# Kernel tuning notes

Hardware: AMD Instinct MI355X
Metric: run time of the kernel (lower is better)

## Reference

```python
import jax, jax.numpy as jnp
import numpy as np

B, H, S, F_RANK, D_HEAD = 1, 8, 4096, 64, 64
NEG = -1e9


def setup_inputs() -> dict:
    key = jax.random.key(0)
    k1, k2, k3, k4 = jax.random.split(key, 4)
    v = jax.random.normal(k1, (B, H, S, D_HEAD), dtype=jnp.float32)
    A1 = jax.random.normal(k2, (B, H, S, F_RANK), dtype=jnp.float32)
    A2 = jax.random.normal(k3, (B, H, F_RANK, S), dtype=jnp.float32)
    mask = jax.random.randint(k4, (B, 1, S, S), 0, 2, dtype=jnp.int32)
    return {"v": v, "A1": A1, "A2": A2, "mask": mask, "len_q": S}


def reference(v, A1, A2, mask, len_q):
    # Rank-f factorized scores: [B,H,len_q,len_q]
    scores = jnp.einsum('bhsf,bhft->bhst', A1[:, :, :len_q, :], A2[:, :, :, :len_q])
    scores = scores[:mask.shape[0]]
    # masked_fill(mask != 0, -1e9)
    scores = jnp.where(mask[:, :, :len_q, :len_q] != 0, jnp.float32(NEG), scores)
    attn = jax.nn.softmax(scores, axis=-1)  # dropout is identity in eval mode
    output = jnp.einsum('bhst,bhtd->bhsd', attn, v[:, :, :len_q, :])
    return (output, attn)
```

## Files before the change

### kernel.cpp

```cpp
#include <hip/hip_runtime.h>
#include <hip/hip_bf16.h>
#include <stdint.h>

#define S_LEN 4096
#define NHEAD 8
#define L2E   1.44269504088896340736f

typedef __attribute__((ext_vector_type(8))) short bf16x8;
typedef __attribute__((ext_vector_type(4))) float f32x4;
typedef unsigned short u16;
typedef unsigned int   u32;

#define MFMA16(a,b,c) __builtin_amdgcn_mfma_f32_16x16x32_bf16((a),(b),(c),0,0,0)
#define EXP2F(x) __builtin_amdgcn_exp2f((x))

__device__ __forceinline__ void gl_lds16(const void* g, void* l) {
  __builtin_amdgcn_global_load_lds((const __attribute__((address_space(1))) void*)g,
                                   (__attribute__((address_space(3))) void*)l, 16, 0, 0);
}

#define WS_A1HI 0u
#define WS_A1LO (4u<<20)
#define WS_A2HI (8u<<20)
#define WS_A2LO (12u<<20)
#define WS_VHI  (16u<<20)
#define WS_VLO  (20u<<20)
#define WS_BM   (24u<<20)
#define WS_INVL (26u<<20)
#define WS_EXPB (28u<<20)

__global__ void pk_mask(const int* __restrict__ mask, u32* __restrict__ bmT) {
  const int sb = blockIdx.x >> 4;
  const int t  = (blockIdx.x & 15) * 256 + threadIdx.x;
  u32 w = 0;
  #pragma unroll
  for (int j = 0; j < 32; ++j)
    w |= (mask[(size_t)(sb * 32 + j) * S_LEN + t] != 0 ? 1u : 0u) << j;
  bmT[sb * S_LEN + t] = w;
}

__global__ void pk_split(const float* __restrict__ src, u16* __restrict__ hi, u16* __restrict__ lo) {
  const int i = blockIdx.x * 256 + threadIdx.x;
  float4 x = ((const float4*)src)[i];
  ushort4 hv, lv;
  #pragma unroll
  for (int j = 0; j < 4; ++j) {
    float xv = ((const float*)&x)[j];
    __hip_bfloat16 hb = __float2bfloat16(xv);
    float hf = __bfloat162float(hb);
    __hip_bfloat16 lb = __float2bfloat16(xv - hf);
    ((u16*)&hv)[j] = *(u16*)&hb;
    ((u16*)&lv)[j] = *(u16*)&lb;
  }
  ((ushort4*)hi)[i] = hv;
  ((ushort4*)lo)[i] = lv;
}

__global__ void pk_tsplit(const float* __restrict__ src, u16* __restrict__ hi, u16* __restrict__ lo,
                          int chunk_stride, int row_stride) {
  const int h = blockIdx.x >> 6, ci = blockIdx.x & 63;
  const float* base = src + (size_t)h * (S_LEN * 64) + (size_t)ci * chunk_stride;
  __shared__ float tile[64][65];
  const int jr = threadIdx.x & 63, ir = threadIdx.x >> 6;
  #pragma unroll
  for (int p = 0; p < 16; ++p) {
    int i = p * 4 + ir;
    tile[i][jr] = base[(size_t)i * row_stride + jr];
  }
  __syncthreads();
  const size_t ob = (size_t)(h * 64 + ci) * 4096;
  #pragma unroll
  for (int p = 0; p < 16; ++p) {
    int o = p * 256 + threadIdx.x;
    int r = o >> 6;
    int cc = (o & 63) ^ ((r & 7) << 3);
    float xv = tile[cc][r];
    __hip_bfloat16 hb = __float2bfloat16(xv);
    float hf = __bfloat162float(hb);
    __hip_bfloat16 lb = __float2bfloat16(xv - hf);
    hi[ob + o] = *(u16*)&hb;
    lo[ob + o] = *(u16*)&lb;
  }
}

__launch_bounds__(512, 2)
__global__ void fattn_main(const u16* __restrict__ a1hi, const u16* __restrict__ a1lo,
                           const u16* __restrict__ a2hi, const u16* __restrict__ a2lo,
                           const u16* __restrict__ vhi,  const u16* __restrict__ vlo,
                           const u32* __restrict__ bmT,  u16* __restrict__ expb,
                           float* __restrict__ invl,     float* __restrict__ dout) {
  const int h   = blockIdx.x & 7;
  const int sb  = blockIdx.x >> 3;
  const int tid = threadIdx.x;
  const int w = tid >> 6, lane = tid & 63;
  const int g = lane >> 4, c = lane & 15;
  const int wsr = w >> 1;
  const int wth = w & 1;
  const int sbase = sb * 128 + wsr * 32;
  const int sb32  = sb * 4 + wsr;

  __shared__ __align__(16) char smem[87040];
  u16*   atb = (u16*)(smem + 65536);
  float* mll = (float*)(smem + 86016);

  bf16x8 a1f[2][2][2];
  #pragma unroll
  for (int mt = 0; mt < 2; ++mt)
    #pragma unroll
    for (int kk = 0; kk < 2; ++kk) {
      size_t base = (size_t)(h * S_LEN + sbase + mt * 16 + c) * 64 + kk * 32 + g * 8;
      a1f[mt][kk][0] = *(const bf16x8*)(a1hi + base);
      a1f[mt][kk][1] = *(const bf16x8*)(a1lo + base);
    }

  float rl[2][4];
  f32x4 oacc[2][4];
  #pragma unroll
  for (int mt = 0; mt < 2; ++mt) {
    #pragma unroll
    for (int r = 0; r < 4; ++r) rl[mt][r] = 0.f;
    #pragma unroll
    for (int dt = 0; dt < 4; ++dt) oacc[mt][dt] = (f32x4){0.f, 0.f, 0.f, 0.f};
  }

  const u32* bmrow = bmT + (size_t)sb32 * S_LEN;

  auto stage_all = [&](int bufi, int ci) {
    const size_t tb = (size_t)(h * 64 + ci) * 4096;
    char* lb = smem + bufi * 32768;
    const int off = w * 1024 + lane * 16;
    gl_lds16((const char*)(a2hi + tb) + off, lb +         w * 1024);
    gl_lds16((const char*)(a2lo + tb) + off, lb +  8192 + w * 1024);
    gl_lds16((const char*)(vhi  + tb) + off, lb + 16384 + w * 1024);
    gl_lds16((const char*)(vlo  + tb) + off, lb + 24576 + w * 1024);
  };

  stage_all(0, 0);
  __syncthreads();

  #pragma unroll 1
  for (int ci = 0; ci < 64; ++ci) {
    if (ci < 63) stage_all((ci + 1) & 1, ci + 1);

    const u16* base = (const u16*)(smem + (ci & 1) * 32768);

    f32x4 acc[2][2];
    #pragma unroll
    for (int mt = 0; mt < 2; ++mt)
      #pragma unroll
      for (int nt = 0; nt < 2; ++nt) acc[mt][nt] = (f32x4){0.f, 0.f, 0.f, 0.f};
    #pragma unroll
    for (int kk = 0; kk < 2; ++kk)
      #pragma unroll
      for (int nt = 0; nt < 2; ++nt) {
        int eb = (wth * 32 + nt * 16 + c) * 64 + ((kk * 32 + g * 8) ^ ((c & 7) << 3));
        bf16x8 bh = *(const bf16x8*)(base + eb);
        bf16x8 bl = *(const bf16x8*)(base + 4096 + eb);
        #pragma unroll
        for (int mt = 0; mt < 2; ++mt) {
          acc[mt][nt] = MFMA16(a1f[mt][kk][0], bh, acc[mt][nt]);
          acc[mt][nt] = MFMA16(a1f[mt][kk][0], bl, acc[mt][nt]);
          acc[mt][nt] = MFMA16(a1f[mt][kk][1], bh, acc[mt][nt]);
        }
      }

    const u32 mw0 = bmrow[ci * 64 + wth * 32 + c];
    const u32 mw1 = bmrow[ci * 64 + wth * 32 + 16 + c];
    float e[2][2][4];
    #pragma unroll
    for (int mt = 0; mt < 2; ++mt)
      #pragma unroll
      for (int nt = 0; nt < 2; ++nt) {
        const u32 mwv = nt ? mw1 : mw0;
        #pragma unroll
        for (int r = 0; r < 4; ++r) {
          float ex = EXP2F(acc[mt][nt][r] * L2E);
          float ev = ((mwv >> (mt * 16 + g * 4 + r)) & 1u) ? 0.f : ex;
          e[mt][nt][r] = ev;
          rl[mt][r] += ev;
        }
      }

    u16* my = atb + w * 1280;
    #pragma unroll
    for (int mt = 0; mt < 2; ++mt)
      #pragma unroll
      for (int nt = 0; nt < 2; ++nt)
        #pragma unroll
        for (int r = 0; r < 4; ++r) {
          __hip_bfloat16 hb = __float2bfloat16(e[mt][nt][r]);
          my[(mt * 16 + g * 4 + r) * 40 + nt * 16 + c] = *(u16*)&hb;
        }
    bf16x8 af[2];
    #pragma unroll
    for (int mt = 0; mt < 2; ++mt)
      af[mt] = *(const bf16x8*)(my + (mt * 16 + c) * 40 + g * 8);

    #pragma unroll
    for (int mt = 0; mt < 2; ++mt)
      *(bf16x8*)(expb + (size_t)(h * S_LEN + sbase + mt * 16 + c) * S_LEN
                       + ci * 64 + wth * 32 + g * 8) = af[mt];

    #pragma unroll
    for (int dt = 0; dt < 4; ++dt) {
      int ve = (dt * 16 + c) * 64 + ((wth * 32 + g * 8) ^ ((c & 7) << 3));
      bf16x8 bvh = *(const bf16x8*)(base + 8192 + ve);
      bf16x8 bvl = *(const bf16x8*)(base + 12288 + ve);
      #pragma unroll
      for (int mt = 0; mt < 2; ++mt) {
        oacc[mt][dt] = MFMA16(af[mt], bvh, oacc[mt][dt]);
        oacc[mt][dt] = MFMA16(af[mt], bvl, oacc[mt][dt]);
      }
    }

    __syncthreads();
  }

  #pragma unroll
  for (int mt = 0; mt < 2; ++mt)
    #pragma unroll
    for (int r = 0; r < 4; ++r) {
      float s = rl[mt][r];
      #pragma unroll
      for (int off = 1; off < 16; off <<= 1) s += __shfl_xor(s, off);
      rl[mt][r] = s;
    }
  __syncthreads();
  if (c == 0) {
    #pragma unroll
    for (int mt = 0; mt < 2; ++mt)
      #pragma unroll
      for (int r = 0; r < 4; ++r)
        mll[w * 32 + mt * 16 + g * 4 + r] = rl[mt][r];
  }
  __syncthreads();
  float inv[2][4];
  #pragma unroll
  for (int mt = 0; mt < 2; ++mt)
    #pragma unroll
    for (int r = 0; r < 4; ++r) {
      float tot = rl[mt][r] + mll[(w ^ 1) * 32 + mt * 16 + g * 4 + r];
      inv[mt][r] = 1.0f / tot;
    }
  if (wth == 0 && c == 0) {
    #pragma unroll
    for (int mt = 0; mt < 2; ++mt)
      #pragma unroll
      for (int r = 0; r < 4; ++r)
        invl[h * S_LEN + sbase + mt * 16 + g * 4 + r] = inv[mt][r];
  }
  #pragma unroll
  for (int mt = 0; mt < 2; ++mt)
    #pragma unroll
    for (int dt = 0; dt < 4; ++dt)
      #pragma unroll
      for (int r = 0; r < 4; ++r)
        oacc[mt][dt][r] *= inv[mt][r];

  __syncthreads();
  float* outx = (float*)smem;
  if (wth == 1) {
    #pragma unroll
    for (int mt = 0; mt < 2; ++mt)
      #pragma unroll
      for (int dt = 0; dt < 4; ++dt)
        #pragma unroll
        for (int r = 0; r < 4; ++r)
          outx[wsr * 2112 + (mt * 16 + g * 4 + r) * 66 + dt * 16 + c] = oacc[mt][dt][r];
  }
  __syncthreads();
  if (wth == 0) {
    #pragma unroll
    for (int mt = 0; mt < 2; ++mt)
      #pragma unroll
      for (int dt = 0; dt < 4; ++dt)
        #pragma unroll
        for (int r = 0; r < 4; ++r) {
          float vv = oacc[mt][dt][r] + outx[wsr * 2112 + (mt * 16 + g * 4 + r) * 66 + dt * 16 + c];
          int s = sbase + mt * 16 + g * 4 + r;
          dout[(size_t)(h * S_LEN + s) * 64 + dt * 16 + c] = vv;
        }
  }
}

__global__ void attn_norm(const u16* __restrict__ expb, const float* __restrict__ invl,
                          float* __restrict__ aout) {
  const int row = blockIdx.x;
  const float iv = invl[row];
  const u16* src = expb + (size_t)row * S_LEN;
  float* dst = aout + (size_t)row * S_LEN;
  const int t0 = threadIdx.x * 16;
  bf16x8 v0 = *(const bf16x8*)(src + t0);
  bf16x8 v1 = *(const bf16x8*)(src + t0 + 8);
  float4 o[4];
  #pragma unroll
  for (int j = 0; j < 8; ++j) {
    ((float*)o)[j]     = __uint_as_float(((u32)(u16)v0[j]) << 16) * iv;
    ((float*)o)[j + 8] = __uint_as_float(((u32)(u16)v1[j]) << 16) * iv;
  }
  #pragma unroll
  for (int k = 0; k < 4; ++k)
    ((float4*)(dst + t0))[k] = o[k];
}

extern "C" void kernel_launch(void* const* d_in, const int* in_sizes, int n_in,
                              void* d_out, int out_size, void* d_ws, size_t ws_size,
                              hipStream_t stream) {
  (void)in_sizes; (void)n_in; (void)out_size; (void)ws_size;
  const float* v    = (const float*)d_in[0];
  const float* A1   = (const float*)d_in[1];
  const float* A2   = (const float*)d_in[2];
  const int*   mask = (const int*)d_in[3];
  float* out = (float*)d_out;
  char* ws = (char*)d_ws;

  u16* a1hi = (u16*)(ws + WS_A1HI);
  u16* a1lo = (u16*)(ws + WS_A1LO);
  u16* a2hi = (u16*)(ws + WS_A2HI);
  u16* a2lo = (u16*)(ws + WS_A2LO);
  u16* vhi  = (u16*)(ws + WS_VHI);
  u16* vlo  = (u16*)(ws + WS_VLO);
  u32* bmT  = (u32*)(ws + WS_BM);
  float* invl = (float*)(ws + WS_INVL);
  u16* expb = (u16*)(ws + WS_EXPB);

  float* aout = out + (size_t)NHEAD * S_LEN * 64;

  pk_mask  <<<2048, 256, 0, stream>>>(mask, bmT);
  pk_split <<<2048, 256, 0, stream>>>(A1, a1hi, a1lo);
  pk_tsplit<<<512,  256, 0, stream>>>(A2, a2hi, a2lo, 64, 4096);
  pk_tsplit<<<512,  256, 0, stream>>>(v,  vhi,  vlo,  4096, 64);
  fattn_main<<<256, 512, 0, stream>>>(a1hi, a1lo, a2hi, a2lo, vhi, vlo, bmT, expb, invl, out);
  attn_norm<<<NHEAD * S_LEN, 256, 0, stream>>>(expb, invl, aout);
}
```

Baseline: 807.8 us.

## Replace bf16 exp scratch and normalize kernel with two-pass recompute writing fp32 attn

The single attention kernel wrote unnormalized bf16 exponentials to a workspace, and a separate kernel then read them back and scaled them into fp32 attention. The new scheme has a first pass that recomputes scores only to get per-row softmax denominators. A second pass recomputes the scores, normalizes them, and writes fp32 attention directly while also doing the P·V product. This removes the bf16 intermediate write and its read-back, at the cost of computing the QK^T/exp work twice. Shared memory in the second pass grows to about 101 KB to stage fp32 tiles.

Result: no change. 794.3 us (-1.7%).

```diff
diff --git a/kernel.cpp b/kernel.cpp
--- a/kernel.cpp
+++ b/kernel.cpp
@@ -17,6 +17,11 @@
 __device__ __forceinline__ void gl_lds16(const void* g, void* l) {
   __builtin_amdgcn_global_load_lds((const __attribute__((address_space(1))) void*)g,
                                    (__attribute__((address_space(3))) void*)l, 16, 0, 0);
+}
+
+__device__ __forceinline__ short f2bf(float x) {
+  __hip_bfloat16 h = __float2bfloat16(x);
+  return *(short*)&h;
 }
 
 #define WS_A1HI 0u
@@ -27,7 +32,6 @@
 #define WS_VLO  (20u<<20)
 #define WS_BM   (24u<<20)
 #define WS_INVL (26u<<20)
-#define WS_EXPB (28u<<20)
 
 __global__ void pk_mask(const int* __restrict__ mask, u32* __restrict__ bmT) {
   const int sb = blockIdx.x >> 4;
@@ -84,11 +88,9 @@
 }
 
 __launch_bounds__(512, 2)
-__global__ void fattn_main(const u16* __restrict__ a1hi, const u16* __restrict__ a1lo,
-                           const u16* __restrict__ a2hi, const u16* __restrict__ a2lo,
-                           const u16* __restrict__ vhi,  const u16* __restrict__ vlo,
-                           const u32* __restrict__ bmT,  u16* __restrict__ expb,
-                           float* __restrict__ invl,     float* __restrict__ dout) {
+__global__ void fattn_pass1(const u16* __restrict__ a1hi, const u16* __restrict__ a1lo,
+                            const u16* __restrict__ a2hi, const u16* __restrict__ a2lo,
+                            const u32* __restrict__ bmT,  float* __restrict__ invl) {
   const int h   = blockIdx.x & 7;
   const int sb  = blockIdx.x >> 3;
   const int tid = threadIdx.x;
@@ -99,9 +101,8 @@
   const int sbase = sb * 128 + wsr * 32;
   const int sb32  = sb * 4 + wsr;
 
-  __shared__ __align__(16) char smem[87040];
-  u16*   atb = (u16*)(smem + 65536);
-  float* mll = (float*)(smem + 86016);
+  __shared__ __align__(16) char smem[33792];
+  float* mll = (float*)(smem + 32768);
 
   bf16x8 a1f[2][2][2];
   #pragma unroll
@@ -114,16 +115,143 @@
     }
 
   float rl[2][4];
+  #pragma unroll
+  for (int mt = 0; mt < 2; ++mt)
+    #pragma unroll
+    for (int r = 0; r < 4; ++r) rl[mt][r] = 0.f;
+
+  const u32* bmrow = bmT + (size_t)sb32 * S_LEN;
+
+  auto stage2 = [&](int bufi, int ci) {
+    const size_t tb = (size_t)(h * 64 + ci) * 4096;
+    char* lb = smem + bufi * 16384;
+    const int off = w * 1024 + lane * 16;
+    gl_lds16((const char*)(a2hi + tb) + off, lb +        w * 1024);
+    gl_lds16((const char*)(a2lo + tb) + off, lb + 8192 + w * 1024);
+  };
+
+  stage2(0, 0);
+  __syncthreads();
+
+  #pragma unroll 1
+  for (int ci = 0; ci < 64; ++ci) {
+    if (ci < 63) stage2((ci + 1) & 1, ci + 1);
+
+    const u16* base = (const u16*)(smem + (ci & 1) * 16384);
+
+    f32x4 acc[2][2];
+    #pragma unroll
+    for (int mt = 0; mt < 2; ++mt)
+      #pragma unroll
+      for (int nt = 0; nt < 2; ++nt) acc[mt][nt] = (f32x4){0.f, 0.f, 0.f, 0.f};
+    #pragma unroll
+    for (int kk = 0; kk < 2; ++kk)
+      #pragma unroll
+      for (int nt = 0; nt < 2; ++nt) {
+        int eb = (wth * 32 + nt * 16 + c) * 64 + ((kk * 32 + g * 8) ^ ((c & 7) << 3));
+        bf16x8 bh = *(const bf16x8*)(base + eb);
+        bf16x8 bl = *(const bf16x8*)(base + 4096 + eb);
+        #pragma unroll
+        for (int mt = 0; mt < 2; ++mt) {
+          acc[mt][nt] = MFMA16(a1f[mt][kk][0], bh, acc[mt][nt]);
+          acc[mt][nt] = MFMA16(a1f[mt][kk][0], bl, acc[mt][nt]);
+          acc[mt][nt] = MFMA16(a1f[mt][kk][1], bh, acc[mt][nt]);
+        }
+      }
+
+    const u32 mw0 = bmrow[ci * 64 + wth * 32 + c];
+    const u32 mw1 = bmrow[ci * 64 + wth * 32 + 16 + c];
+    #pragma unroll
+    for (int mt = 0; mt < 2; ++mt)
+      #pragma unroll
+      for (int nt = 0; nt < 2; ++nt) {
+        const u32 mwv = nt ? mw1 : mw0;
+        #pragma unroll
+        for (int r = 0; r < 4; ++r) {
+          float ex = EXP2F(acc[mt][nt][r] * L2E);
+          rl[mt][r] += ((mwv >> (mt * 16 + g * 4 + r)) & 1u) ? 0.f : ex;
+        }
+      }
+
+    __syncthreads();
+  }
+
+  #pragma unroll
+  for (int mt = 0; mt < 2; ++mt)
+    #pragma unroll
+    for (int r = 0; r < 4; ++r) {
+      float s = rl[mt][r];
+      #pragma unroll
+      for (int off = 1; off < 16; off <<= 1) s += __shfl_xor(s, off);
+      rl[mt][r] = s;
+    }
+  __syncthreads();
+  if (c == 0) {
+    #pragma unroll
+    for (int mt = 0; mt < 2; ++mt)
+      #pragma unroll
+      for (int r = 0; r < 4; ++r)
+        mll[w * 32 + mt * 16 + g * 4 + r] = rl[mt][r];
+  }
+  __syncthreads();
+  if (wth == 0 && c == 0) {
+    #pragma unroll
+    for (int mt = 0; mt < 2; ++mt)
+      #pragma unroll
+      for (int r = 0; r < 4; ++r) {
+        float tot = rl[mt][r] + mll[(w ^ 1) * 32 + mt * 16 + g * 4 + r];
+        invl[h * S_LEN + sbase + mt * 16 + g * 4 + r] = 1.0f / tot;
+      }
+  }
+}
+
+__launch_bounds__(512, 2)
+__global__ void fattn_pass2(const u16* __restrict__ a1hi, const u16* __restrict__ a1lo,
+                            const u16* __restrict__ a2hi, const u16* __restrict__ a2lo,
+                            const u16* __restrict__ vhi,  const u16* __restrict__ vlo,
+                            const u32* __restrict__ bmT,  const float* __restrict__ invl,
+                            float* __restrict__ dout) {
+  const int h   = blockIdx.x & 7;
+  const int sb  = blockIdx.x >> 3;
+  const int tid = threadIdx.x;
+  const int w = tid >> 6, lane = tid & 63;
+  const int g = lane >> 4, c = lane & 15;
+  const int wsr = w >> 1;
+  const int wth = w & 1;
+  const int sbase = sb * 128 + wsr * 32;
+  const int sb32  = sb * 4 + wsr;
+
+  __shared__ __align__(16) char smem[103424];
+  float* atbf = (float*)(smem + 65536);
+  float* mll  = (float*)(smem + 102400);
+  (void)mll;
+
+  bf16x8 a1f[2][2][2];
+  #pragma unroll
+  for (int mt = 0; mt < 2; ++mt)
+    #pragma unroll
+    for (int kk = 0; kk < 2; ++kk) {
+      size_t base = (size_t)(h * S_LEN + sbase + mt * 16 + c) * 64 + kk * 32 + g * 8;
+      a1f[mt][kk][0] = *(const bf16x8*)(a1hi + base);
+      a1f[mt][kk][1] = *(const bf16x8*)(a1lo + base);
+    }
+
+  float inv[2][4];
+  #pragma unroll
+  for (int mt = 0; mt < 2; ++mt)
+    #pragma unroll
+    for (int r = 0; r < 4; ++r)
+      inv[mt][r] = invl[h * S_LEN + sbase + mt * 16 + g * 4 + r];
+
   f32x4 oacc[2][4];
   #pragma unroll
-  for (int mt = 0; mt < 2; ++mt) {
-    #pragma unroll
-    for (int r = 0; r < 4; ++r) rl[mt][r] = 0.f;
+  for (int mt = 0; mt < 2; ++mt)
     #pragma unroll
     for (int dt = 0; dt < 4; ++dt) oacc[mt][dt] = (f32x4){0.f, 0.f, 0.f, 0.f};
-  }
 
   const u32* bmrow = bmT + (size_t)sb32 * S_LEN;
+  float* aout = dout + (size_t)NHEAD * S_LEN * 64;
+  float* myatb = atbf + w * 1152;
 
   auto stage_all = [&](int bufi, int ci) {
     const size_t tb = (size_t)(h * 64 + ci) * 4096;
@@ -166,7 +294,6 @@
 
     const u32 mw0 = bmrow[ci * 64 + wth * 32 + c];
     const u32 mw1 = bmrow[ci * 64 + wth * 32 + 16 + c];
-    float e[2][2][4];
     #pragma unroll
     for (int mt = 0; mt < 2; ++mt)
       #pragma unroll
@@ -175,31 +302,33 @@
         #pragma unroll
         for (int r = 0; r < 4; ++r) {
           float ex = EXP2F(acc[mt][nt][r] * L2E);
-          float ev = ((mwv >> (mt * 16 + g * 4 + r)) & 1u) ? 0.f : ex;
-          e[mt][nt][r] = ev;
-          rl[mt][r] += ev;
+          float av = ((mwv >> (mt * 16 + g * 4 + r)) & 1u) ? 0.f : ex * inv[mt][r];
+          myatb[(mt * 16 + g * 4 + r) * 36 + nt * 16 + c] = av;
         }
       }
 
-    u16* my = atb + w * 1280;
-    #pragma unroll
-    for (int mt = 0; mt < 2; ++mt)
-      #pragma unroll
-      for (int nt = 0; nt < 2; ++nt)
-        #pragma unroll
-        for (int r = 0; r < 4; ++r) {
-          __hip_bfloat16 hb = __float2bfloat16(e[mt][nt][r]);
-          my[(mt * 16 + g * 4 + r) * 40 + nt * 16 + c] = *(u16*)&hb;
-        }
+    asm volatile("" ::: "memory");
+
     bf16x8 af[2];
     #pragma unroll
-    for (int mt = 0; mt < 2; ++mt)
-      af[mt] = *(const bf16x8*)(my + (mt * 16 + c) * 40 + g * 8);
-
-    #pragma unroll
-    for (int mt = 0; mt < 2; ++mt)
-      *(bf16x8*)(expb + (size_t)(h * S_LEN + sbase + mt * 16 + c) * S_LEN
-                       + ci * 64 + wth * 32 + g * 8) = af[mt];
+    for (int mt = 0; mt < 2; ++mt) {
+      const float* arow = myatb + (mt * 16 + c) * 36 + g * 8;
+      float4 f0 = *(const float4*)(arow);
+      float4 f1 = *(const float4*)(arow + 4);
+      af[mt][0] = f2bf(f0.x); af[mt][1] = f2bf(f0.y);
+      af[mt][2] = f2bf(f0.z); af[mt][3] = f2bf(f0.w);
+      af[mt][4] = f2bf(f1.x); af[mt][5] = f2bf(f1.y);
+      af[mt][6] = f2bf(f1.z); af[mt][7] = f2bf(f1.w);
+    }
+
+    {
+      const size_t rb = (size_t)(h * S_LEN + sbase) * S_LEN + ci * 64 + wth * 32;
+      #pragma unroll
+      for (int i = 0; i < 8; ++i) {
+        float2 vv = *(const float2*)(myatb + (i * 4 + g) * 36 + 2 * c);
+        *(float2*)(aout + rb + (size_t)(i * 4 + g) * S_LEN + 2 * c) = vv;
+      }
+    }
 
     #pragma unroll
     for (int dt = 0; dt < 4; ++dt) {
@@ -215,47 +344,6 @@
 
     __syncthreads();
   }
-
-  #pragma unroll
-  for (int mt = 0; mt < 2; ++mt)
-    #pragma unroll
-    for (int r = 0; r < 4; ++r) {
-      float s = rl[mt][r];
-      #pragma unroll
-      for (int off = 1; off < 16; off <<= 1) s += __shfl_xor(s, off);
-      rl[mt][r] = s;
-    }
-  __syncthreads();
-  if (c == 0) {
-    #pragma unroll
-    for (int mt = 0; mt < 2; ++mt)
-      #pragma unroll
-      for (int r = 0; r < 4; ++r)
-        mll[w * 32 + mt * 16 + g * 4 + r] = rl[mt][r];
-  }
-  __syncthreads();
-  float inv[2][4];
-  #pragma unroll
-  for (int mt = 0; mt < 2; ++mt)
-    #pragma unroll
-    for (int r = 0; r < 4; ++r) {
-      float tot = rl[mt][r] + mll[(w ^ 1) * 32 + mt * 16 + g * 4 + r];
-      inv[mt][r] = 1.0f / tot;
-    }
-  if (wth == 0 && c == 0) {
-    #pragma unroll
-    for (int mt = 0; mt < 2; ++mt)
-      #pragma unroll
-      for (int r = 0; r < 4; ++r)
-        invl[h * S_LEN + sbase + mt * 16 + g * 4 + r] = inv[mt][r];
-  }
-  #pragma unroll
-  for (int mt = 0; mt < 2; ++mt)
-    #pragma unroll
-    for (int dt = 0; dt < 4; ++dt)
-      #pragma unroll
-      for (int r = 0; r < 4; ++r)
-        oacc[mt][dt][r] *= inv[mt][r];
 
   __syncthreads();
   float* outx = (float*)smem;
@@ -281,26 +369,6 @@
           dout[(size_t)(h * S_LEN + s) * 64 + dt * 16 + c] = vv;
         }
   }
-}
-
-__global__ void attn_norm(const u16* __restrict__ expb, const float* __restrict__ invl,
-                          float* __restrict__ aout) {
-  const int row = blockIdx.x;
-  const float iv = invl[row];
-  const u16* src = expb + (size_t)row * S_LEN;
-  float* dst = aout + (size_t)row * S_LEN;
-  const int t0 = threadIdx.x * 16;
-  bf16x8 v0 = *(const bf16x8*)(src + t0);
-  bf16x8 v1 = *(const bf16x8*)(src + t0 + 8);
-  float4 o[4];
-  #pragma unroll
-  for (int j = 0; j < 8; ++j) {
-    ((float*)o)[j]     = __uint_as_float(((u32)(u16)v0[j]) << 16) * iv;
-    ((float*)o)[j + 8] = __uint_as_float(((u32)(u16)v1[j]) << 16) * iv;
-  }
-  #pragma unroll
-  for (int k = 0; k < 4; ++k)
-    ((float4*)(dst + t0))[k] = o[k];
 }
 
 extern "C" void kernel_launch(void* const* d_in, const int* in_sizes, int n_in,
@@ -322,14 +390,11 @@
   u16* vlo  = (u16*)(ws + WS_VLO);
   u32* bmT  = (u32*)(ws + WS_BM);
   float* invl = (float*)(ws + WS_INVL);
-  u16* expb = (u16*)(ws + WS_EXPB);
-
-  float* aout = out + (size_t)NHEAD * S_LEN * 64;
 
   pk_mask  <<<2048, 256, 0, stream>>>(mask, bmT);
   pk_split <<<2048, 256, 0, stream>>>(A1, a1hi, a1lo);
   pk_tsplit<<<512,  256, 0, stream>>>(A2, a2hi, a2lo, 64, 4096);
   pk_tsplit<<<512,  256, 0, stream>>>(v,  vhi,  vlo,  4096, 64);
-  fattn_main<<<256, 512, 0, stream>>>(a1hi, a1lo, a2hi, a2lo, vhi, vlo, bmT, expb, invl, out);
-  attn_norm<<<NHEAD * S_LEN, 256, 0, stream>>>(expb, invl, aout);
-}
+  fattn_pass1<<<256, 512, 0, stream>>>(a1hi, a1lo, a2hi, a2lo, bmT, invl);
+  fattn_pass2<<<256, 512, 0, stream>>>(a1hi, a1lo, a2hi, a2lo, vhi, vlo, bmT, invl, out);
+}
```
